# Kernel optimization log

Measured on AMD Instinct MI355X. Metric: run time of the kernel, lower is better.

Reference implementation:

```python
import jax, jax.numpy as jnp
import numpy as np

E, H, I, B, K = 8, 2048, 5632, 1024, 2


def setup_inputs() -> dict:
    key = jax.random.key(0)
    k_x, k_id, k_w, k_g, k_u, k_d = jax.random.split(key, 6)
    x = jax.random.normal(k_x, (B, H), dtype=jnp.float32)
    expert_ids = jax.random.randint(k_id, (B, K), 0, E).astype(jnp.int32)
    ew = jax.random.uniform(k_w, (B, K), dtype=jnp.float32)
    expert_weights = ew / jnp.sum(ew, axis=-1, keepdims=True)  # router probs, sum to 1
    scale = 0.02
    gate_weights = jax.random.normal(k_g, (E, H, I), dtype=jnp.float32) * scale
    up_weights = jax.random.normal(k_u, (E, H, I), dtype=jnp.float32) * scale
    down_weights = jax.random.normal(k_d, (E, I, H), dtype=jnp.float32) * scale
    return {
        "x": x,
        "expert_ids": expert_ids,
        "expert_weights": expert_weights,
        "gate_weights": gate_weights,
        "up_weights": up_weights,
        "down_weights": down_weights,
    }


def reference(x, expert_ids, expert_weights, gate_weights, up_weights, down_weights):
    # Faithful math: per token t, expert e = expert_ids[t,k]:
    #   out[t] = sum_k expert_weights[t,k] * (silu(x W_gate_e) * (x W_up_e)) W_down_e
    # Implemented as dense all-expert GEMMs + select, which computes the
    # identical per-expert matmuls as the original's gathered-weight einsums
    # without materializing the [B,K,H,I] gathered weight tensor.
    gate_all = jnp.einsum('bh,ehi->bei', x, gate_weights)        # [B,E,I]
    up_all = jnp.einsum('bh,ehi->bei', x, up_weights)            # [B,E,I]
    act_all = jax.nn.silu(gate_all) * up_all                     # [B,E,I]
    out_all = jnp.einsum('bei,eih->beh', act_all, down_weights)  # [B,E,H]
    # Select the top_k experts' outputs per token: [B,K,H]
    sel = jnp.take_along_axis(out_all, expert_ids[:, :, None], axis=1)
    return jnp.sum(sel * expert_weights[:, :, None], axis=1)     # [B,H]
```

## Files before the change

kernel.cpp:

```cpp
#include <hip/hip_runtime.h>
#include <hip/hip_bf16.h>

#define E_ 8
#define H_ 2048
#define I_ 5632
#define B_ 1024
#define K_ 2
#define NROWS (B_*K_)

#define BM 128
#define BN 64
#define BK 64
#define MAXT 24
#define NKG (H_/BK)
#define NKD (I_/BK)
#define NYG (I_/BN)
#define NYD (H_/BN)

typedef __attribute__((ext_vector_type(8))) __bf16 bf16x8;
typedef __attribute__((ext_vector_type(4))) float f32x4;

union BF4 { __bf16 b[4]; uint2 q; };
union BF8 { __bf16 b[8]; uint4 q; };

__device__ __forceinline__ void gld_lds16(const void* g, void* l) {
  __builtin_amdgcn_global_load_lds(
      (const __attribute__((address_space(1))) void*)g,
      (__attribute__((address_space(3))) void*)l, 16, 0, 0);
}

#define GLOAD4(dst, ptr) asm volatile("global_load_dwordx4 %0, %1, off" : "=v"(dst) : "v"(ptr))
#define WAITV(N) do { asm volatile("s_waitcnt vmcnt(" #N ")" ::: "memory"); __builtin_amdgcn_sched_barrier(0); } while(0)
#define WAITL()  do { asm volatile("s_waitcnt lgkmcnt(0)" ::: "memory"); __builtin_amdgcn_sched_barrier(0); } while(0)
#define BAR()    __builtin_amdgcn_s_barrier()

#define MSK(c) (((c)&7) ^ (((c)>>2)&7))

__global__ void cvtx_kernel(const float* __restrict__ x, __bf16* __restrict__ xb) {
  int i = (blockIdx.x * 256 + threadIdx.x) * 8;
  float4 a = *(const float4*)(x + i);
  float4 b = *(const float4*)(x + i + 4);
  BF8 r;
  r.b[0] = (__bf16)a.x; r.b[1] = (__bf16)a.y; r.b[2] = (__bf16)a.z; r.b[3] = (__bf16)a.w;
  r.b[4] = (__bf16)b.x; r.b[5] = (__bf16)b.y; r.b[6] = (__bf16)b.z; r.b[7] = (__bf16)b.w;
  *(uint4*)(xb + i) = r.q;
}

__global__ void route_kernel(const int* __restrict__ ids,
                             int* __restrict__ counts, int* __restrict__ offsets,
                             int* __restrict__ tlist, int* __restrict__ row_of,
                             int* __restrict__ tile_e, int* __restrict__ tile_m) {
  __shared__ int sc[E_], sp[E_], so[E_];
  int t = threadIdx.x;
  if (t < E_) { sc[t] = 0; sp[t] = 0; }
  __syncthreads();
  for (int idx = t; idx < NROWS; idx += 256) atomicAdd(&sc[ids[idx]], 1);
  __syncthreads();
  if (t == 0) {
    int acc = 0;
    for (int e = 0; e < E_; ++e) { so[e] = acc; acc += sc[e]; }
    int nt = 0;
    for (int e = 0; e < E_; ++e)
      for (int m0 = 0; m0 < sc[e]; m0 += BM) { tile_e[nt] = e; tile_m[nt] = m0; ++nt; }
    for (; nt < MAXT; ++nt) { tile_e[nt] = 0; tile_m[nt] = 0x7FFFFFFF; }
  }
  __syncthreads();
  for (int idx = t; idx < NROWS; idx += 256) {
    int e = ids[idx];
    int slot = atomicAdd(&sp[e], 1);
    int row = so[e] + slot;
    tlist[row] = idx / K_;
    row_of[idx] = row;
  }
  if (t < E_) { counts[t] = sc[t]; offsets[t] = so[t]; }
}

__global__ __launch_bounds__(256, 2) void gateup_kernel(
    const __bf16* __restrict__ xb, const float* __restrict__ gw,
    const float* __restrict__ uw, const int* __restrict__ counts,
    const int* __restrict__ offsets, const int* __restrict__ tlist,
    const int* __restrict__ tile_e, const int* __restrict__ tile_m,
    __bf16* __restrict__ act)
{
  extern __shared__ char smem[];
  char* As0 = smem;
  char* As1 = smem + 16384;
  char* Bg0 = smem + 32768;
  char* Bg1 = smem + 40960;
  char* Bu0 = smem + 49152;
  char* Bu1 = smem + 57344;

  const int id = blockIdx.x;
  const int w  = (id & 7) * 264 + (id >> 3);
  const int tt = w % MAXT;
  const int ny = w / MAXT;
  const int e  = tile_e[tt];
  const int m0 = tile_m[tt];
  const int cnt = counts[e];
  if (m0 >= cnt) return;
  const int off = offsets[e];
  const int n0 = ny * BN;

  const int tid  = threadIdx.x;
  const int lane = tid & 63;
  const int wave = tid >> 6;
  const int wr = (wave >> 1) * 64;
  const int wc = (wave & 1) * 32;

  const __bf16* asrc0; const __bf16* asrc1; const __bf16* asrc2; const __bf16* asrc3;
  int ad0, ad1, ad2, ad3;
  {
    const __bf16* s[4]; int d[4];
#pragma unroll
    for (int i = 0; i < 4; ++i) {
      int f = i*256 + tid;
      int r = f >> 3, cs = f & 7;
      int rr = m0 + r; if (rr >= cnt) rr = cnt - 1;
      int tok = tlist[off + rr];
      s[i] = xb + (size_t)tok * H_ + ((cs ^ (r & 7)) << 3);
      d[i] = f * 16;
    }
    asrc0=s[0]; asrc1=s[1]; asrc2=s[2]; asrc3=s[3];
    ad0=d[0]; ad1=d[1]; ad2=d[2]; ad3=d[3];
  }

  const int cq = tid & 15;
  const int kb = (tid >> 4) * 4;
  const float* pg0 = gw + ((size_t)e*H_ + kb + 0)*I_ + n0 + 4*cq;
  const float* pg1 = gw + ((size_t)e*H_ + kb + 1)*I_ + n0 + 4*cq;
  const float* pg2 = gw + ((size_t)e*H_ + kb + 2)*I_ + n0 + 4*cq;
  const float* pg3 = gw + ((size_t)e*H_ + kb + 3)*I_ + n0 + 4*cq;
  const float* pu0 = uw + ((size_t)e*H_ + kb + 0)*I_ + n0 + 4*cq;
  const float* pu1 = uw + ((size_t)e*H_ + kb + 1)*I_ + n0 + 4*cq;
  const float* pu2 = uw + ((size_t)e*H_ + kb + 2)*I_ + n0 + 4*cq;
  const float* pu3 = uw + ((size_t)e*H_ + kb + 3)*I_ + n0 + 4*cq;
  const int slot = kb >> 3;
  const int half = (kb & 4) << 1;
  int bw0, bw1, bw2, bw3;
  {
    int b[4];
#pragma unroll
    for (int i = 0; i < 4; ++i) {
      int c = 4*cq + i;
      b[i] = c*128 + ((slot ^ MSK(c)) << 4) + half;
    }
    bw0=b[0]; bw1=b[1]; bw2=b[2]; bw3=b[3];
  }

  f32x4 vgA_0,vgA_1,vgA_2,vgA_3, vuA_0,vuA_1,vuA_2,vuA_3;
  f32x4 vgB_0,vgB_1,vgB_2,vgB_3, vuB_0,vuB_1,vuB_2,vuB_3;

  f32x4 accg[4][2], accu[4][2];
#pragma unroll
  for (int i = 0; i < 4; ++i)
#pragma unroll
    for (int j = 0; j < 2; ++j) {
      accg[i][j] = (f32x4){0.f,0.f,0.f,0.f};
      accu[i][j] = (f32x4){0.f,0.f,0.f,0.f};
    }

  auto COMPUTE = [&](const char* Ab, const char* Bgb, const char* Bub) {
#pragma unroll
    for (int kk = 0; kk < 2; ++kk) {
      const int ks = kk*4 + (lane >> 4);
      const int r0 = wr + (lane & 15);
      const int swa = (ks ^ (r0 & 7)) << 4;
      bf16x8 a0 = *(const bf16x8*)(Ab + (r0 +  0)*128 + swa);
      bf16x8 a1 = *(const bf16x8*)(Ab + (r0 + 16)*128 + swa);
      bf16x8 a2 = *(const bf16x8*)(Ab + (r0 + 32)*128 + swa);
      bf16x8 a3 = *(const bf16x8*)(Ab + (r0 + 48)*128 + swa);
      const int c0 = wc + (lane & 15);
      const int swb0 = (ks ^ MSK(c0)) << 4;
      const int swb1 = swb0 ^ (4 << 4);
      bf16x8 g0 = *(const bf16x8*)(Bgb + c0*128 + swb0);
      bf16x8 g1 = *(const bf16x8*)(Bgb + (c0+16)*128 + swb1);
      bf16x8 u0 = *(const bf16x8*)(Bub + c0*128 + swb0);
      bf16x8 u1 = *(const bf16x8*)(Bub + (c0+16)*128 + swb1);
      accg[0][0] = __builtin_amdgcn_mfma_f32_16x16x32_bf16(a0, g0, accg[0][0], 0,0,0);
      accg[1][0] = __builtin_amdgcn_mfma_f32_16x16x32_bf16(a1, g0, accg[1][0], 0,0,0);
      accg[2][0] = __builtin_amdgcn_mfma_f32_16x16x32_bf16(a2, g0, accg[2][0], 0,0,0);
      accg[3][0] = __builtin_amdgcn_mfma_f32_16x16x32_bf16(a3, g0, accg[3][0], 0,0,0);
      accg[0][1] = __builtin_amdgcn_mfma_f32_16x16x32_bf16(a0, g1, accg[0][1], 0,0,0);
      accg[1][1] = __builtin_amdgcn_mfma_f32_16x16x32_bf16(a1, g1, accg[1][1], 0,0,0);
      accg[2][1] = __builtin_amdgcn_mfma_f32_16x16x32_bf16(a2, g1, accg[2][1], 0,0,0);
      accg[3][1] = __builtin_amdgcn_mfma_f32_16x16x32_bf16(a3, g1, accg[3][1], 0,0,0);
      accu[0][0] = __builtin_amdgcn_mfma_f32_16x16x32_bf16(a0, u0, accu[0][0], 0,0,0);
      accu[1][0] = __builtin_amdgcn_mfma_f32_16x16x32_bf16(a1, u0, accu[1][0], 0,0,0);
      accu[2][0] = __builtin_amdgcn_mfma_f32_16x16x32_bf16(a2, u0, accu[2][0], 0,0,0);
      accu[3][0] = __builtin_amdgcn_mfma_f32_16x16x32_bf16(a3, u0, accu[3][0], 0,0,0);
      accu[0][1] = __builtin_amdgcn_mfma_f32_16x16x32_bf16(a0, u1, accu[0][1], 0,0,0);
      accu[1][1] = __builtin_amdgcn_mfma_f32_16x16x32_bf16(a1, u1, accu[1][1], 0,0,0);
      accu[2][1] = __builtin_amdgcn_mfma_f32_16x16x32_bf16(a2, u1, accu[2][1], 0,0,0);
      accu[3][1] = __builtin_amdgcn_mfma_f32_16x16x32_bf16(a3, u1, accu[3][1], 0,0,0);
    }
  };

#define GU_PF(S, KPF) do { size_t o_ = (size_t)(KPF)*(size_t)BK*(size_t)I_; \
    GLOAD4(vg##S##_0, pg0+o_); GLOAD4(vu##S##_0, pu0+o_); \
    GLOAD4(vg##S##_1, pg1+o_); GLOAD4(vu##S##_1, pu1+o_); \
    GLOAD4(vg##S##_2, pg2+o_); GLOAD4(vu##S##_2, pu2+o_); \
    GLOAD4(vg##S##_3, pg3+o_); GLOAD4(vu##S##_3, pu3+o_); } while(0)

#define GU_CVW1(BG, V0, V1, V2, V3, BWI, I) do { BF4 p_; \
    p_.b[0]=(__bf16)V0[I]; p_.b[1]=(__bf16)V1[I]; p_.b[2]=(__bf16)V2[I]; p_.b[3]=(__bf16)V3[I]; \
    *(uint2*)((BG)+BWI) = p_.q; } while(0)

#define GU_CVW(S, BG, BU) do { \
    GU_CVW1(BG, vg##S##_0, vg##S##_1, vg##S##_2, vg##S##_3, bw0, 0); \
    GU_CVW1(BG, vg##S##_0, vg##S##_1, vg##S##_2, vg##S##_3, bw1, 1); \
    GU_CVW1(BG, vg##S##_0, vg##S##_1, vg##S##_2, vg##S##_3, bw2, 2); \
    GU_CVW1(BG, vg##S##_0, vg##S##_1, vg##S##_2, vg##S##_3, bw3, 3); \
    GU_CVW1(BU, vu##S##_0, vu##S##_1, vu##S##_2, vu##S##_3, bw0, 0); \
    GU_CVW1(BU, vu##S##_0, vu##S##_1, vu##S##_2, vu##S##_3, bw1, 1); \
    GU_CVW1(BU, vu##S##_0, vu##S##_1, vu##S##_2, vu##S##_3, bw2, 2); \
    GU_CVW1(BU, vu##S##_0, vu##S##_1, vu##S##_2, vu##S##_3, bw3, 3); } while(0)

#define GU_GLDA(DST, KPF) do { size_t k_ = (size_t)(KPF)*(size_t)BK; \
    gld_lds16(asrc0 + k_, (DST)+ad0); gld_lds16(asrc1 + k_, (DST)+ad1); \
    gld_lds16(asrc2 + k_, (DST)+ad2); gld_lds16(asrc3 + k_, (DST)+ad3); } while(0)

  GU_PF(A, 0);
  GU_GLDA(As0, 0);
  WAITV(4);
  GU_CVW(A, Bg0, Bu0);
  GU_PF(B, 1);
  GU_GLDA(As1, 1);
  WAITV(12);
  WAITL();
  BAR();

#pragma unroll 1
  for (int kt = 0; kt < NKG; kt += 2) {
    {
      int kpf = kt + 2; if (kpf > NKG-1) kpf = NKG-1;
      GU_PF(A, kpf);
      COMPUTE(As0, Bg0, Bu0);
      WAITV(12);
      GU_CVW(B, Bg1, Bu1);
      WAITV(8);
      WAITL();
      BAR();
      GU_GLDA(As0, kpf);
    }
    {
      int kpf = kt + 3; if (kpf > NKG-1) kpf = NKG-1;
      GU_PF(B, kpf);
      COMPUTE(As1, Bg1, Bu1);
      WAITV(12);
      GU_CVW(A, Bg0, Bu0);
      WAITV(8);
      WAITL();
      BAR();
      GU_GLDA(As1, kpf);
    }
  }
  WAITV(0);
  WAITL();

  const int rsub = (lane >> 4) * 4;
  const int csub = lane & 15;
#pragma unroll
  for (int mi = 0; mi < 4; ++mi)
#pragma unroll
    for (int j = 0; j < 4; ++j) {
      int rl = wr + mi*16 + rsub + j;
      if (m0 + rl < cnt) {
        size_t orow = (size_t)(off + m0 + rl) * I_ + n0 + wc + csub;
#pragma unroll
        for (int cg = 0; cg < 2; ++cg) {
          float g = accg[mi][cg][j];
          float u = accu[mi][cg][j];
          float sg = g / (1.0f + __expf(-g));
          act[orow + cg*16] = (__bf16)(sg * u);
        }
      }
    }
#undef GU_PF
#undef GU_CVW
#undef GU_CVW1
#undef GU_GLDA
}

__global__ __launch_bounds__(256, 3) void down_kernel(
    const __bf16* __restrict__ act, const float* __restrict__ dw,
    const int* __restrict__ counts, const int* __restrict__ offsets,
    const int* __restrict__ tile_e, const int* __restrict__ tile_m,
    float* __restrict__ rowbuf)
{
  extern __shared__ char smem[];
  char* As0 = smem;
  char* As1 = smem + 16384;
  char* Bs0 = smem + 32768;
  char* Bs1 = smem + 40960;

  const int id = blockIdx.x;
  const int w  = (id & 7) * 96 + (id >> 3);
  const int tt = w % MAXT;
  const int ny = w / MAXT;
  const int e  = tile_e[tt];
  const int m0 = tile_m[tt];
  const int cnt = counts[e];
  if (m0 >= cnt) return;
  const int off = offsets[e];
  const int n0 = ny * BN;

  const int tid  = threadIdx.x;
  const int lane = tid & 63;
  const int wave = tid >> 6;
  const int wr = (wave >> 1) * 64;
  const int wc = (wave & 1) * 32;

  const __bf16* asrc0; const __bf16* asrc1; const __bf16* asrc2; const __bf16* asrc3;
  int ad0, ad1, ad2, ad3;
  {
    const __bf16* s[4]; int d[4];
#pragma unroll
    for (int i = 0; i < 4; ++i) {
      int f = i*256 + tid;
      int r = f >> 3, cs = f & 7;
      int rr = m0 + r; if (rr >= cnt) rr = cnt - 1;
      s[i] = act + (size_t)(off + rr) * I_ + ((cs ^ (r & 7)) << 3);
      d[i] = f * 16;
    }
    asrc0=s[0]; asrc1=s[1]; asrc2=s[2]; asrc3=s[3];
    ad0=d[0]; ad1=d[1]; ad2=d[2]; ad3=d[3];
  }

  const int cq = tid & 15;
  const int kb = (tid >> 4) * 4;
  const float* pd0 = dw + ((size_t)e*I_ + kb + 0)*H_ + n0 + 4*cq;
  const float* pd1 = dw + ((size_t)e*I_ + kb + 1)*H_ + n0 + 4*cq;
  const float* pd2 = dw + ((size_t)e*I_ + kb + 2)*H_ + n0 + 4*cq;
  const float* pd3 = dw + ((size_t)e*I_ + kb + 3)*H_ + n0 + 4*cq;
  const int slot = kb >> 3;
  const int half = (kb & 4) << 1;
  int bw0, bw1, bw2, bw3;
  {
    int b[4];
#pragma unroll
    for (int i = 0; i < 4; ++i) {
      int c = 4*cq + i;
      b[i] = c*128 + ((slot ^ MSK(c)) << 4) + half;
    }
    bw0=b[0]; bw1=b[1]; bw2=b[2]; bw3=b[3];
  }

  f32x4 vdA_0,vdA_1,vdA_2,vdA_3;
  f32x4 vdB_0,vdB_1,vdB_2,vdB_3;

  f32x4 acc[4][2];
#pragma unroll
  for (int i = 0; i < 4; ++i)
#pragma unroll
    for (int j = 0; j < 2; ++j) acc[i][j] = (f32x4){0.f,0.f,0.f,0.f};

  auto COMPUTE = [&](const char* Ab, const char* Bb) {
#pragma unroll
    for (int kk = 0; kk < 2; ++kk) {
      const int ks = kk*4 + (lane >> 4);
      const int r0 = wr + (lane & 15);
      const int swa = (ks ^ (r0 & 7)) << 4;
      bf16x8 a0 = *(const bf16x8*)(Ab + (r0 +  0)*128 + swa);
      bf16x8 a1 = *(const bf16x8*)(Ab + (r0 + 16)*128 + swa);
      bf16x8 a2 = *(const bf16x8*)(Ab + (r0 + 32)*128 + swa);
      bf16x8 a3 = *(const bf16x8*)(Ab + (r0 + 48)*128 + swa);
      const int c0 = wc + (lane & 15);
      const int swb0 = (ks ^ MSK(c0)) << 4;
      const int swb1 = swb0 ^ (4 << 4);
      bf16x8 b0 = *(const bf16x8*)(Bb + c0*128 + swb0);
      bf16x8 b1 = *(const bf16x8*)(Bb + (c0+16)*128 + swb1);
      acc[0][0] = __builtin_amdgcn_mfma_f32_16x16x32_bf16(a0, b0, acc[0][0], 0,0,0);
      acc[1][0] = __builtin_amdgcn_mfma_f32_16x16x32_bf16(a1, b0, acc[1][0], 0,0,0);
      acc[2][0] = __builtin_amdgcn_mfma_f32_16x16x32_bf16(a2, b0, acc[2][0], 0,0,0);
      acc[3][0] = __builtin_amdgcn_mfma_f32_16x16x32_bf16(a3, b0, acc[3][0], 0,0,0);
      acc[0][1] = __builtin_amdgcn_mfma_f32_16x16x32_bf16(a0, b1, acc[0][1], 0,0,0);
      acc[1][1] = __builtin_amdgcn_mfma_f32_16x16x32_bf16(a1, b1, acc[1][1], 0,0,0);
      acc[2][1] = __builtin_amdgcn_mfma_f32_16x16x32_bf16(a2, b1, acc[2][1], 0,0,0);
      acc[3][1] = __builtin_amdgcn_mfma_f32_16x16x32_bf16(a3, b1, acc[3][1], 0,0,0);
    }
  };

#define DN_PF(S, KPF) do { size_t o_ = (size_t)(KPF)*(size_t)BK*(size_t)H_; \
    GLOAD4(vd##S##_0, pd0+o_); GLOAD4(vd##S##_1, pd1+o_); \
    GLOAD4(vd##S##_2, pd2+o_); GLOAD4(vd##S##_3, pd3+o_); } while(0)

#define DN_CVW1(BB, V0, V1, V2, V3, BWI, I) do { BF4 p_; \
    p_.b[0]=(__bf16)V0[I]; p_.b[1]=(__bf16)V1[I]; p_.b[2]=(__bf16)V2[I]; p_.b[3]=(__bf16)V3[I]; \
    *(uint2*)((BB)+BWI) = p_.q; } while(0)

#define DN_CVW(S, BB) do { \
    DN_CVW1(BB, vd##S##_0, vd##S##_1, vd##S##_2, vd##S##_3, bw0, 0); \
    DN_CVW1(BB, vd##S##_0, vd##S##_1, vd##S##_2, vd##S##_3, bw1, 1); \
    DN_CVW1(BB, vd##S##_0, vd##S##_1, vd##S##_2, vd##S##_3, bw2, 2); \
    DN_CVW1(BB, vd##S##_0, vd##S##_1, vd##S##_2, vd##S##_3, bw3, 3); } while(0)

#define DN_GLDA(DST, KPF) do { size_t k_ = (size_t)(KPF)*(size_t)BK; \
    gld_lds16(asrc0 + k_, (DST)+ad0); gld_lds16(asrc1 + k_, (DST)+ad1); \
    gld_lds16(asrc2 + k_, (DST)+ad2); gld_lds16(asrc3 + k_, (DST)+ad3); } while(0)

  DN_PF(A, 0);
  DN_GLDA(As0, 0);
  WAITV(4);
  DN_CVW(A, Bs0);
  DN_PF(B, 1);
  DN_GLDA(As1, 1);
  WAITV(8);
  WAITL();
  BAR();

#pragma unroll 1
  for (int kt = 0; kt < NKD; kt += 2) {
    {
      int kpf = kt + 2; if (kpf > NKD-1) kpf = NKD-1;
      DN_PF(A, kpf);
      COMPUTE(As0, Bs0);
      WAITV(8);
      DN_CVW(B, Bs1);
      WAITV(4);
      WAITL();
      BAR();
      DN_GLDA(As0, kpf);
    }
    {
      int kpf = kt + 3; if (kpf > NKD-1) kpf = NKD-1;
      DN_PF(B, kpf);
      COMPUTE(As1, Bs1);
      WAITV(8);
      DN_CVW(A, Bs0);
      WAITV(4);
      WAITL();
      BAR();
      DN_GLDA(As1, kpf);
    }
  }
  WAITV(0);
  WAITL();

  const int rsub = (lane >> 4) * 4;
  const int csub = lane & 15;
#pragma unroll
  for (int mi = 0; mi < 4; ++mi)
#pragma unroll
    for (int j = 0; j < 4; ++j) {
      int rl = wr + mi*16 + rsub + j;
      if (m0 + rl < cnt) {
        size_t orow = (size_t)(off + m0 + rl) * H_ + n0 + wc + csub;
#pragma unroll
        for (int cg = 0; cg < 2; ++cg)
          rowbuf[orow + cg*16] = acc[mi][cg][j];
      }
    }
#undef DN_PF
#undef DN_CVW
#undef DN_CVW1
#undef DN_GLDA
}

__global__ void combine_kernel(const float* __restrict__ ew, const int* __restrict__ row_of,
                               const float* __restrict__ rowbuf, float* __restrict__ out) {
  int idx = blockIdx.x * 256 + threadIdx.x;
  int t  = idx >> 9;
  int h4 = idx & 511;
  float w0 = ew[t*2+0], w1 = ew[t*2+1];
  int r0 = row_of[t*2+0], r1 = row_of[t*2+1];
  float4 a = *(const float4*)(rowbuf + (size_t)r0*H_ + h4*4);
  float4 b = *(const float4*)(rowbuf + (size_t)r1*H_ + h4*4);
  float4 o;
  o.x = w0*a.x + w1*b.x; o.y = w0*a.y + w1*b.y;
  o.z = w0*a.z + w1*b.z; o.w = w0*a.w + w1*b.w;
  *(float4*)(out + (size_t)idx*4) = o;
}

extern "C" void kernel_launch(void* const* d_in, const int* in_sizes, int n_in,
                              void* d_out, int out_size, void* d_ws, size_t ws_size,
                              hipStream_t stream) {
  const float* x   = (const float*)d_in[0];
  const int*   ids = (const int*)d_in[1];
  const float* ew  = (const float*)d_in[2];
  const float* gw  = (const float*)d_in[3];
  const float* uw  = (const float*)d_in[4];
  const float* dwn = (const float*)d_in[5];
  float* out = (float*)d_out;

  char* ws = (char*)d_ws;
  int* counts  = (int*)ws;
  int* offsets = counts + 8;
  int* tlist   = offsets + 8;
  int* row_of  = tlist + NROWS;
  int* tile_e  = row_of + NROWS;
  int* tile_m  = tile_e + MAXT;
  __bf16* xb   = (__bf16*)(ws + 32768);
  __bf16* act  = (__bf16*)(ws + 32768 + (size_t)B_*H_*2);
  float* rowbuf = (float*)(ws + 32768 + (size_t)B_*H_*2 + (size_t)NROWS*I_*2);

  hipFuncSetAttribute(reinterpret_cast<const void*>(&gateup_kernel),
                      hipFuncAttributeMaxDynamicSharedMemorySize, 65536);
  hipFuncSetAttribute(reinterpret_cast<const void*>(&down_kernel),
                      hipFuncAttributeMaxDynamicSharedMemorySize, 49152);

  cvtx_kernel<<<B_*H_/(256*8), 256, 0, stream>>>(x, xb);
  route_kernel<<<1, 256, 0, stream>>>(ids, counts, offsets, tlist, row_of, tile_e, tile_m);

  gateup_kernel<<<MAXT*NYG, 256, 65536, stream>>>(xb, gw, uw, counts, offsets, tlist,
                                                  tile_e, tile_m, act);

  down_kernel<<<MAXT*NYD, 256, 49152, stream>>>(act, dwn, counts, offsets,
                                                tile_e, tile_m, rowbuf);

  combine_kernel<<<(B_*H_/4)/256, 256, 0, stream>>>(ew, row_of, rowbuf, out);
}
```

Baseline: 415.1 us.

## Load A fragments directly into registers and narrow gate/up tile width

```diff
diff --git a/kernel.cpp b/kernel.cpp
--- a/kernel.cpp
+++ b/kernel.cpp
@@ -9,30 +9,25 @@
 #define NROWS (B_*K_)
 
 #define BM 128
-#define BN 64
 #define BK 64
 #define MAXT 24
 #define NKG (H_/BK)
 #define NKD (I_/BK)
-#define NYG (I_/BN)
-#define NYD (H_/BN)
+#define NYG (I_/32)
+#define NYD (H_/64)
 
 typedef __attribute__((ext_vector_type(8))) __bf16 bf16x8;
 typedef __attribute__((ext_vector_type(4))) float f32x4;
 
+union BF2 { __bf16 b[2]; uint q; };
 union BF4 { __bf16 b[4]; uint2 q; };
 union BF8 { __bf16 b[8]; uint4 q; };
-
-__device__ __forceinline__ void gld_lds16(const void* g, void* l) {
-  __builtin_amdgcn_global_load_lds(
-      (const __attribute__((address_space(1))) void*)g,
-      (__attribute__((address_space(3))) void*)l, 16, 0, 0);
-}
 
 #define GLOAD4(dst, ptr) asm volatile("global_load_dwordx4 %0, %1, off" : "=v"(dst) : "v"(ptr))
 #define WAITV(N) do { asm volatile("s_waitcnt vmcnt(" #N ")" ::: "memory"); __builtin_amdgcn_sched_barrier(0); } while(0)
 #define WAITL()  do { asm volatile("s_waitcnt lgkmcnt(0)" ::: "memory"); __builtin_amdgcn_sched_barrier(0); } while(0)
 #define BAR()    __builtin_amdgcn_s_barrier()
+#define SB0()    __builtin_amdgcn_sched_barrier(0)
 
 #define MSK(c) (((c)&7) ^ (((c)>>2)&7))
 
@@ -83,15 +78,13 @@
     __bf16* __restrict__ act)
 {
   extern __shared__ char smem[];
-  char* As0 = smem;
-  char* As1 = smem + 16384;
-  char* Bg0 = smem + 32768;
-  char* Bg1 = smem + 40960;
-  char* Bu0 = smem + 49152;
-  char* Bu1 = smem + 57344;
+  char* Bg0 = smem;
+  char* Bg1 = smem + 4096;
+  char* Bu0 = smem + 8192;
+  char* Bu1 = smem + 12288;
 
   const int id = blockIdx.x;
-  const int w  = (id & 7) * 264 + (id >> 3);
+  const int w  = (id & 7) * 528 + (id >> 3);
   const int tt = w % MAXT;
   const int ny = w / MAXT;
   const int e  = tile_e[tt];
@@ -99,133 +92,120 @@
   const int cnt = counts[e];
   if (m0 >= cnt) return;
   const int off = offsets[e];
-  const int n0 = ny * BN;
+  const int n0 = ny * 32;
 
   const int tid  = threadIdx.x;
   const int lane = tid & 63;
   const int wave = tid >> 6;
   const int wr = (wave >> 1) * 64;
-  const int wc = (wave & 1) * 32;
-
-  const __bf16* asrc0; const __bf16* asrc1; const __bf16* asrc2; const __bf16* asrc3;
-  int ad0, ad1, ad2, ad3;
+  const int wc = (wave & 1) * 16;
+
+  const __bf16* ab0; const __bf16* ab1; const __bf16* ab2; const __bf16* ab3;
   {
-    const __bf16* s[4]; int d[4];
-#pragma unroll
-    for (int i = 0; i < 4; ++i) {
-      int f = i*256 + tid;
-      int r = f >> 3, cs = f & 7;
-      int rr = m0 + r; if (rr >= cnt) rr = cnt - 1;
+    const __bf16* a[4];
+#pragma unroll
+    for (int mi = 0; mi < 4; ++mi) {
+      int rr = m0 + wr + mi*16 + (lane & 15);
+      if (rr >= cnt) rr = cnt - 1;
       int tok = tlist[off + rr];
-      s[i] = xb + (size_t)tok * H_ + ((cs ^ (r & 7)) << 3);
-      d[i] = f * 16;
-    }
-    asrc0=s[0]; asrc1=s[1]; asrc2=s[2]; asrc3=s[3];
-    ad0=d[0]; ad1=d[1]; ad2=d[2]; ad3=d[3];
-  }
-
-  const int cq = tid & 15;
-  const int kb = (tid >> 4) * 4;
-  const float* pg0 = gw + ((size_t)e*H_ + kb + 0)*I_ + n0 + 4*cq;
-  const float* pg1 = gw + ((size_t)e*H_ + kb + 1)*I_ + n0 + 4*cq;
-  const float* pg2 = gw + ((size_t)e*H_ + kb + 2)*I_ + n0 + 4*cq;
-  const float* pg3 = gw + ((size_t)e*H_ + kb + 3)*I_ + n0 + 4*cq;
-  const float* pu0 = uw + ((size_t)e*H_ + kb + 0)*I_ + n0 + 4*cq;
-  const float* pu1 = uw + ((size_t)e*H_ + kb + 1)*I_ + n0 + 4*cq;
-  const float* pu2 = uw + ((size_t)e*H_ + kb + 2)*I_ + n0 + 4*cq;
-  const float* pu3 = uw + ((size_t)e*H_ + kb + 3)*I_ + n0 + 4*cq;
-  const int slot = kb >> 3;
-  const int half = (kb & 4) << 1;
+      a[mi] = xb + (size_t)tok * H_ + ((lane >> 4) * 8);
+    }
+    ab0=a[0]; ab1=a[1]; ab2=a[2]; ab3=a[3];
+  }
+
+  const int q  = tid & 7;
+  const int kr = tid >> 3;
+  const int kb = kr * 2;
+  const float* pg0 = gw + ((size_t)e*H_ + kb + 0)*I_ + n0 + 4*q;
+  const float* pg1 = gw + ((size_t)e*H_ + kb + 1)*I_ + n0 + 4*q;
+  const float* pu0 = uw + ((size_t)e*H_ + kb + 0)*I_ + n0 + 4*q;
+  const float* pu1 = uw + ((size_t)e*H_ + kb + 1)*I_ + n0 + 4*q;
+  const int slot = kr >> 2;
+  const int insl = (kr & 3) * 4;
   int bw0, bw1, bw2, bw3;
   {
     int b[4];
 #pragma unroll
     for (int i = 0; i < 4; ++i) {
-      int c = 4*cq + i;
-      b[i] = c*128 + ((slot ^ MSK(c)) << 4) + half;
+      int c = 4*q + i;
+      b[i] = c*128 + ((slot ^ MSK(c)) << 4) + insl;
     }
     bw0=b[0]; bw1=b[1]; bw2=b[2]; bw3=b[3];
   }
 
-  f32x4 vgA_0,vgA_1,vgA_2,vgA_3, vuA_0,vuA_1,vuA_2,vuA_3;
-  f32x4 vgB_0,vgB_1,vgB_2,vgB_3, vuB_0,vuB_1,vuB_2,vuB_3;
-
-  f32x4 accg[4][2], accu[4][2];
-#pragma unroll
-  for (int i = 0; i < 4; ++i)
-#pragma unroll
-    for (int j = 0; j < 2; ++j) {
-      accg[i][j] = (f32x4){0.f,0.f,0.f,0.f};
-      accu[i][j] = (f32x4){0.f,0.f,0.f,0.f};
-    }
-
-  auto COMPUTE = [&](const char* Ab, const char* Bgb, const char* Bub) {
-#pragma unroll
-    for (int kk = 0; kk < 2; ++kk) {
-      const int ks = kk*4 + (lane >> 4);
-      const int r0 = wr + (lane & 15);
-      const int swa = (ks ^ (r0 & 7)) << 4;
-      bf16x8 a0 = *(const bf16x8*)(Ab + (r0 +  0)*128 + swa);
-      bf16x8 a1 = *(const bf16x8*)(Ab + (r0 + 16)*128 + swa);
-      bf16x8 a2 = *(const bf16x8*)(Ab + (r0 + 32)*128 + swa);
-      bf16x8 a3 = *(const bf16x8*)(Ab + (r0 + 48)*128 + swa);
+  f32x4 vgA_0,vgA_1, vuA_0,vuA_1;
+  f32x4 vgB_0,vgB_1, vuB_0,vuB_1;
+  bf16x8 tA_0,tA_1,tA_2,tA_3,tA_4,tA_5,tA_6,tA_7;
+
+  f32x4 accg[4], accu[4];
+#pragma unroll
+  for (int i = 0; i < 4; ++i) {
+    accg[i] = (f32x4){0.f,0.f,0.f,0.f};
+    accu[i] = (f32x4){0.f,0.f,0.f,0.f};
+  }
+
+  auto COMPUTE = [&](const char* Bgp, const char* Bup) {
+    {
+      const int ks = (lane >> 4);
       const int c0 = wc + (lane & 15);
-      const int swb0 = (ks ^ MSK(c0)) << 4;
-      const int swb1 = swb0 ^ (4 << 4);
-      bf16x8 g0 = *(const bf16x8*)(Bgb + c0*128 + swb0);
-      bf16x8 g1 = *(const bf16x8*)(Bgb + (c0+16)*128 + swb1);
-      bf16x8 u0 = *(const bf16x8*)(Bub + c0*128 + swb0);
-      bf16x8 u1 = *(const bf16x8*)(Bub + (c0+16)*128 + swb1);
-      accg[0][0] = __builtin_amdgcn_mfma_f32_16x16x32_bf16(a0, g0, accg[0][0], 0,0,0);
-      accg[1][0] = __builtin_amdgcn_mfma_f32_16x16x32_bf16(a1, g0, accg[1][0], 0,0,0);
-      accg[2][0] = __builtin_amdgcn_mfma_f32_16x16x32_bf16(a2, g0, accg[2][0], 0,0,0);
-      accg[3][0] = __builtin_amdgcn_mfma_f32_16x16x32_bf16(a3, g0, accg[3][0], 0,0,0);
-      accg[0][1] = __builtin_amdgcn_mfma_f32_16x16x32_bf16(a0, g1, accg[0][1], 0,0,0);
-      accg[1][1] = __builtin_amdgcn_mfma_f32_16x16x32_bf16(a1, g1, accg[1][1], 0,0,0);
-      accg[2][1] = __builtin_amdgcn_mfma_f32_16x16x32_bf16(a2, g1, accg[2][1], 0,0,0);
-      accg[3][1] = __builtin_amdgcn_mfma_f32_16x16x32_bf16(a3, g1, accg[3][1], 0,0,0);
-      accu[0][0] = __builtin_amdgcn_mfma_f32_16x16x32_bf16(a0, u0, accu[0][0], 0,0,0);
-      accu[1][0] = __builtin_amdgcn_mfma_f32_16x16x32_bf16(a1, u0, accu[1][0], 0,0,0);
-      accu[2][0] = __builtin_amdgcn_mfma_f32_16x16x32_bf16(a2, u0, accu[2][0], 0,0,0);
-      accu[3][0] = __builtin_amdgcn_mfma_f32_16x16x32_bf16(a3, u0, accu[3][0], 0,0,0);
-      accu[0][1] = __builtin_amdgcn_mfma_f32_16x16x32_bf16(a0, u1, accu[0][1], 0,0,0);
-      accu[1][1] = __builtin_amdgcn_mfma_f32_16x16x32_bf16(a1, u1, accu[1][1], 0,0,0);
-      accu[2][1] = __builtin_amdgcn_mfma_f32_16x16x32_bf16(a2, u1, accu[2][1], 0,0,0);
-      accu[3][1] = __builtin_amdgcn_mfma_f32_16x16x32_bf16(a3, u1, accu[3][1], 0,0,0);
+      const int swb = (ks ^ MSK(c0)) << 4;
+      bf16x8 g0 = *(const bf16x8*)(Bgp + c0*128 + swb);
+      bf16x8 u0 = *(const bf16x8*)(Bup + c0*128 + swb);
+      accg[0] = __builtin_amdgcn_mfma_f32_16x16x32_bf16(tA_0, g0, accg[0], 0,0,0);
+      accg[1] = __builtin_amdgcn_mfma_f32_16x16x32_bf16(tA_1, g0, accg[1], 0,0,0);
+      accg[2] = __builtin_amdgcn_mfma_f32_16x16x32_bf16(tA_2, g0, accg[2], 0,0,0);
+      accg[3] = __builtin_amdgcn_mfma_f32_16x16x32_bf16(tA_3, g0, accg[3], 0,0,0);
+      accu[0] = __builtin_amdgcn_mfma_f32_16x16x32_bf16(tA_0, u0, accu[0], 0,0,0);
+      accu[1] = __builtin_amdgcn_mfma_f32_16x16x32_bf16(tA_1, u0, accu[1], 0,0,0);
+      accu[2] = __builtin_amdgcn_mfma_f32_16x16x32_bf16(tA_2, u0, accu[2], 0,0,0);
+      accu[3] = __builtin_amdgcn_mfma_f32_16x16x32_bf16(tA_3, u0, accu[3], 0,0,0);
+    }
+    {
+      const int ks = 4 + (lane >> 4);
+      const int c0 = wc + (lane & 15);
+      const int swb = (ks ^ MSK(c0)) << 4;
+      bf16x8 g1 = *(const bf16x8*)(Bgp + c0*128 + swb);
+      bf16x8 u1 = *(const bf16x8*)(Bup + c0*128 + swb);
+      accg[0] = __builtin_amdgcn_mfma_f32_16x16x32_bf16(tA_4, g1, accg[0], 0,0,0);
+      accg[1] = __builtin_amdgcn_mfma_f32_16x16x32_bf16(tA_5, g1, accg[1], 0,0,0);
+      accg[2] = __builtin_amdgcn_mfma_f32_16x16x32_bf16(tA_6, g1, accg[2], 0,0,0);
+      accg[3] = __builtin_amdgcn_mfma_f32_16x16x32_bf16(tA_7, g1, accg[3], 0,0,0);
+      accu[0] = __builtin_amdgcn_mfma_f32_16x16x32_bf16(tA_4, u1, accu[0], 0,0,0);
+      accu[1] = __builtin_amdgcn_mfma_f32_16x16x32_bf16(tA_5, u1, accu[1], 0,0,0);
+      accu[2] = __builtin_amdgcn_mfma_f32_16x16x32_bf16(tA_6, u1, accu[2], 0,0,0);
+      accu[3] = __builtin_amdgcn_mfma_f32_16x16x32_bf16(tA_7, u1, accu[3], 0,0,0);
     }
   };
 
 #define GU_PF(S, KPF) do { size_t o_ = (size_t)(KPF)*(size_t)BK*(size_t)I_; \
-    GLOAD4(vg##S##_0, pg0+o_); GLOAD4(vu##S##_0, pu0+o_); \
-    GLOAD4(vg##S##_1, pg1+o_); GLOAD4(vu##S##_1, pu1+o_); \
-    GLOAD4(vg##S##_2, pg2+o_); GLOAD4(vu##S##_2, pu2+o_); \
-    GLOAD4(vg##S##_3, pg3+o_); GLOAD4(vu##S##_3, pu3+o_); } while(0)
-
-#define GU_CVW1(BG, V0, V1, V2, V3, BWI, I) do { BF4 p_; \
-    p_.b[0]=(__bf16)V0[I]; p_.b[1]=(__bf16)V1[I]; p_.b[2]=(__bf16)V2[I]; p_.b[3]=(__bf16)V3[I]; \
-    *(uint2*)((BG)+BWI) = p_.q; } while(0)
+    GLOAD4(vg##S##_0, pg0+o_); GLOAD4(vg##S##_1, pg1+o_); \
+    GLOAD4(vu##S##_0, pu0+o_); GLOAD4(vu##S##_1, pu1+o_); } while(0)
+
+#define GU_CVW1(BB, V0, V1, BWI, I) do { BF2 p_; \
+    p_.b[0]=(__bf16)V0[I]; p_.b[1]=(__bf16)V1[I]; \
+    *(uint*)((BB)+BWI) = p_.q; } while(0)
 
 #define GU_CVW(S, BG, BU) do { \
-    GU_CVW1(BG, vg##S##_0, vg##S##_1, vg##S##_2, vg##S##_3, bw0, 0); \
-    GU_CVW1(BG, vg##S##_0, vg##S##_1, vg##S##_2, vg##S##_3, bw1, 1); \
-    GU_CVW1(BG, vg##S##_0, vg##S##_1, vg##S##_2, vg##S##_3, bw2, 2); \
-    GU_CVW1(BG, vg##S##_0, vg##S##_1, vg##S##_2, vg##S##_3, bw3, 3); \
-    GU_CVW1(BU, vu##S##_0, vu##S##_1, vu##S##_2, vu##S##_3, bw0, 0); \
-    GU_CVW1(BU, vu##S##_0, vu##S##_1, vu##S##_2, vu##S##_3, bw1, 1); \
-    GU_CVW1(BU, vu##S##_0, vu##S##_1, vu##S##_2, vu##S##_3, bw2, 2); \
-    GU_CVW1(BU, vu##S##_0, vu##S##_1, vu##S##_2, vu##S##_3, bw3, 3); } while(0)
-
-#define GU_GLDA(DST, KPF) do { size_t k_ = (size_t)(KPF)*(size_t)BK; \
-    gld_lds16(asrc0 + k_, (DST)+ad0); gld_lds16(asrc1 + k_, (DST)+ad1); \
-    gld_lds16(asrc2 + k_, (DST)+ad2); gld_lds16(asrc3 + k_, (DST)+ad3); } while(0)
+    GU_CVW1(BG, vg##S##_0, vg##S##_1, bw0, 0); \
+    GU_CVW1(BG, vg##S##_0, vg##S##_1, bw1, 1); \
+    GU_CVW1(BG, vg##S##_0, vg##S##_1, bw2, 2); \
+    GU_CVW1(BG, vg##S##_0, vg##S##_1, bw3, 3); \
+    GU_CVW1(BU, vu##S##_0, vu##S##_1, bw0, 0); \
+    GU_CVW1(BU, vu##S##_0, vu##S##_1, bw1, 1); \
+    GU_CVW1(BU, vu##S##_0, vu##S##_1, bw2, 2); \
+    GU_CVW1(BU, vu##S##_0, vu##S##_1, bw3, 3); } while(0)
+
+#define APF(KT) do { size_t e0_ = (size_t)(KT)*64; \
+    GLOAD4(tA_0, ab0 + e0_);      GLOAD4(tA_1, ab1 + e0_); \
+    GLOAD4(tA_2, ab2 + e0_);      GLOAD4(tA_3, ab3 + e0_); \
+    GLOAD4(tA_4, ab0 + e0_ + 32); GLOAD4(tA_5, ab1 + e0_ + 32); \
+    GLOAD4(tA_6, ab2 + e0_ + 32); GLOAD4(tA_7, ab3 + e0_ + 32); } while(0)
 
   GU_PF(A, 0);
-  GU_GLDA(As0, 0);
-  WAITV(4);
+  WAITV(0);
   GU_CVW(A, Bg0, Bu0);
   GU_PF(B, 1);
-  GU_GLDA(As1, 1);
-  WAITV(12);
+  APF(0);
   WAITL();
   BAR();
 
@@ -234,24 +214,25 @@
     {
       int kpf = kt + 2; if (kpf > NKG-1) kpf = NKG-1;
       GU_PF(A, kpf);
-      COMPUTE(As0, Bg0, Bu0);
-      WAITV(12);
+      WAITV(4);
+      COMPUTE(Bg0, Bu0);
       GU_CVW(B, Bg1, Bu1);
-      WAITV(8);
+      SB0();
+      APF(kt + 1);
       WAITL();
       BAR();
-      GU_GLDA(As0, kpf);
     }
     {
       int kpf = kt + 3; if (kpf > NKG-1) kpf = NKG-1;
+      int ka  = kt + 2; if (ka  > NKG-1) ka  = NKG-1;
       GU_PF(B, kpf);
-      COMPUTE(As1, Bg1, Bu1);
-      WAITV(12);
+      WAITV(4);
+      COMPUTE(Bg1, Bu1);
       GU_CVW(A, Bg0, Bu0);
-      WAITV(8);
+      SB0();
+      APF(ka);
       WAITL();
       BAR();
-      GU_GLDA(As1, kpf);
     }
   }
   WAITV(0);
@@ -266,32 +247,27 @@
       int rl = wr + mi*16 + rsub + j;
       if (m0 + rl < cnt) {
         size_t orow = (size_t)(off + m0 + rl) * I_ + n0 + wc + csub;
-#pragma unroll
-        for (int cg = 0; cg < 2; ++cg) {
-          float g = accg[mi][cg][j];
-          float u = accu[mi][cg][j];
-          float sg = g / (1.0f + __expf(-g));
-          act[orow + cg*16] = (__bf16)(sg * u);
-        }
+        float g = accg[mi][j];
+        float u = accu[mi][j];
+        float sg = g / (1.0f + __expf(-g));
+        act[orow] = (__bf16)(sg * u);
       }
     }
 #undef GU_PF
 #undef GU_CVW
 #undef GU_CVW1
-#undef GU_GLDA
-}
-
-__global__ __launch_bounds__(256, 3) void down_kernel(
+#undef APF
+}
+
+__global__ __launch_bounds__(256, 2) void down_kernel(
     const __bf16* __restrict__ act, const float* __restrict__ dw,
     const int* __restrict__ counts, const int* __restrict__ offsets,
     const int* __restrict__ tile_e, const int* __restrict__ tile_m,
     float* __restrict__ rowbuf)
 {
   extern __shared__ char smem[];
-  char* As0 = smem;
-  char* As1 = smem + 16384;
-  char* Bs0 = smem + 32768;
-  char* Bs1 = smem + 40960;
+  char* Bs0 = smem;
+  char* Bs1 = smem + 8192;
 
   const int id = blockIdx.x;
   const int w  = (id & 7) * 96 + (id >> 3);
@@ -302,7 +278,7 @@
   const int cnt = counts[e];
   if (m0 >= cnt) return;
   const int off = offsets[e];
-  const int n0 = ny * BN;
+  const int n0 = ny * 64;
 
   const int tid  = threadIdx.x;
   const int lane = tid & 63;
@@ -310,20 +286,16 @@
   const int wr = (wave >> 1) * 64;
   const int wc = (wave & 1) * 32;
 
-  const __bf16* asrc0; const __bf16* asrc1; const __bf16* asrc2; const __bf16* asrc3;
-  int ad0, ad1, ad2, ad3;
+  const __bf16* ab0; const __bf16* ab1; const __bf16* ab2; const __bf16* ab3;
   {
-    const __bf16* s[4]; int d[4];
-#pragma unroll
-    for (int i = 0; i < 4; ++i) {
-      int f = i*256 + tid;
-      int r = f >> 3, cs = f & 7;
-      int rr = m0 + r; if (rr >= cnt) rr = cnt - 1;
-      s[i] = act + (size_t)(off + rr) * I_ + ((cs ^ (r & 7)) << 3);
-      d[i] = f * 16;
-    }
-    asrc0=s[0]; asrc1=s[1]; asrc2=s[2]; asrc3=s[3];
-    ad0=d[0]; ad1=d[1]; ad2=d[2]; ad3=d[3];
+    const __bf16* a[4];
+#pragma unroll
+    for (int mi = 0; mi < 4; ++mi) {
+      int rr = m0 + wr + mi*16 + (lane & 15);
+      if (rr >= cnt) rr = cnt - 1;
+      a[mi] = act + (size_t)(off + rr) * I_ + ((lane >> 4) * 8);
+    }
+    ab0=a[0]; ab1=a[1]; ab2=a[2]; ab3=a[3];
   }
 
   const int cq = tid & 15;
@@ -347,6 +319,7 @@
 
   f32x4 vdA_0,vdA_1,vdA_2,vdA_3;
   f32x4 vdB_0,vdB_1,vdB_2,vdB_3;
+  bf16x8 tA_0,tA_1,tA_2,tA_3,tA_4,tA_5,tA_6,tA_7;
 
   f32x4 acc[4][2];
 #pragma unroll
@@ -354,29 +327,38 @@
 #pragma unroll
     for (int j = 0; j < 2; ++j) acc[i][j] = (f32x4){0.f,0.f,0.f,0.f};
 
-  auto COMPUTE = [&](const char* Ab, const char* Bb) {
-#pragma unroll
-    for (int kk = 0; kk < 2; ++kk) {
-      const int ks = kk*4 + (lane >> 4);
-      const int r0 = wr + (lane & 15);
-      const int swa = (ks ^ (r0 & 7)) << 4;
-      bf16x8 a0 = *(const bf16x8*)(Ab + (r0 +  0)*128 + swa);
-      bf16x8 a1 = *(const bf16x8*)(Ab + (r0 + 16)*128 + swa);
-      bf16x8 a2 = *(const bf16x8*)(Ab + (r0 + 32)*128 + swa);
-      bf16x8 a3 = *(const bf16x8*)(Ab + (r0 + 48)*128 + swa);
+  auto COMPUTE = [&](const char* Bp) {
+    {
+      const int ks = (lane >> 4);
       const int c0 = wc + (lane & 15);
       const int swb0 = (ks ^ MSK(c0)) << 4;
       const int swb1 = swb0 ^ (4 << 4);
-      bf16x8 b0 = *(const bf16x8*)(Bb + c0*128 + swb0);
-      bf16x8 b1 = *(const bf16x8*)(Bb + (c0+16)*128 + swb1);
-      acc[0][0] = __builtin_amdgcn_mfma_f32_16x16x32_bf16(a0, b0, acc[0][0], 0,0,0);
-      acc[1][0] = __builtin_amdgcn_mfma_f32_16x16x32_bf16(a1, b0, acc[1][0], 0,0,0);
-      acc[2][0] = __builtin_amdgcn_mfma_f32_16x16x32_bf16(a2, b0, acc[2][0], 0,0,0);
-      acc[3][0] = __builtin_amdgcn_mfma_f32_16x16x32_bf16(a3, b0, acc[3][0], 0,0,0);
-      acc[0][1] = __builtin_amdgcn_mfma_f32_16x16x32_bf16(a0, b1, acc[0][1], 0,0,0);
-      acc[1][1] = __builtin_amdgcn_mfma_f32_16x16x32_bf16(a1, b1, acc[1][1], 0,0,0);
-      acc[2][1] = __builtin_amdgcn_mfma_f32_16x16x32_bf16(a2, b1, acc[2][1], 0,0,0);
-      acc[3][1] = __builtin_amdgcn_mfma_f32_16x16x32_bf16(a3, b1, acc[3][1], 0,0,0);
+      bf16x8 b0 = *(const bf16x8*)(Bp + c0*128 + swb0);
+      bf16x8 b1 = *(const bf16x8*)(Bp + (c0+16)*128 + swb1);
+      acc[0][0] = __builtin_amdgcn_mfma_f32_16x16x32_bf16(tA_0, b0, acc[0][0], 0,0,0);
+      acc[1][0] = __builtin_amdgcn_mfma_f32_16x16x32_bf16(tA_1, b0, acc[1][0], 0,0,0);
+      acc[2][0] = __builtin_amdgcn_mfma_f32_16x16x32_bf16(tA_2, b0, acc[2][0], 0,0,0);
+      acc[3][0] = __builtin_amdgcn_mfma_f32_16x16x32_bf16(tA_3, b0, acc[3][0], 0,0,0);
+      acc[0][1] = __builtin_amdgcn_mfma_f32_16x16x32_bf16(tA_0, b1, acc[0][1], 0,0,0);
+      acc[1][1] = __builtin_amdgcn_mfma_f32_16x16x32_bf16(tA_1, b1, acc[1][1], 0,0,0);
+      acc[2][1] = __builtin_amdgcn_mfma_f32_16x16x32_bf16(tA_2, b1, acc[2][1], 0,0,0);
+      acc[3][1] = __builtin_amdgcn_mfma_f32_16x16x32_bf16(tA_3, b1, acc[3][1], 0,0,0);
+    }
+    {
+      const int ks = 4 + (lane >> 4);
+      const int c0 = wc + (lane & 15);
+      const int swb0 = (ks ^ MSK(c0)) << 4;
+      const int swb1 = swb0 ^ (4 << 4);
+      bf16x8 b0 = *(const bf16x8*)(Bp + c0*128 + swb0);
+      bf16x8 b1 = *(const bf16x8*)(Bp + (c0+16)*128 + swb1);
+      acc[0][0] = __builtin_amdgcn_mfma_f32_16x16x32_bf16(tA_4, b0, acc[0][0], 0,0,0);
+      acc[1][0] = __builtin_amdgcn_mfma_f32_16x16x32_bf16(tA_5, b0, acc[1][0], 0,0,0);
+      acc[2][0] = __builtin_amdgcn_mfma_f32_16x16x32_bf16(tA_6, b0, acc[2][0], 0,0,0);
+      acc[3][0] = __builtin_amdgcn_mfma_f32_16x16x32_bf16(tA_7, b0, acc[3][0], 0,0,0);
+      acc[0][1] = __builtin_amdgcn_mfma_f32_16x16x32_bf16(tA_4, b1, acc[0][1], 0,0,0);
+      acc[1][1] = __builtin_amdgcn_mfma_f32_16x16x32_bf16(tA_5, b1, acc[1][1], 0,0,0);
+      acc[2][1] = __builtin_amdgcn_mfma_f32_16x16x32_bf16(tA_6, b1, acc[2][1], 0,0,0);
+      acc[3][1] = __builtin_amdgcn_mfma_f32_16x16x32_bf16(tA_7, b1, acc[3][1], 0,0,0);
     }
   };
 
@@ -394,17 +376,17 @@
     DN_CVW1(BB, vd##S##_0, vd##S##_1, vd##S##_2, vd##S##_3, bw2, 2); \
     DN_CVW1(BB, vd##S##_0, vd##S##_1, vd##S##_2, vd##S##_3, bw3, 3); } while(0)
 
-#define DN_GLDA(DST, KPF) do { size_t k_ = (size_t)(KPF)*(size_t)BK; \
-    gld_lds16(asrc0 + k_, (DST)+ad0); gld_lds16(asrc1 + k_, (DST)+ad1); \
-    gld_lds16(asrc2 + k_, (DST)+ad2); gld_lds16(asrc3 + k_, (DST)+ad3); } while(0)
+#define APF(KT) do { size_t e0_ = (size_t)(KT)*64; \
+    GLOAD4(tA_0, ab0 + e0_);      GLOAD4(tA_1, ab1 + e0_); \
+    GLOAD4(tA_2, ab2 + e0_);      GLOAD4(tA_3, ab3 + e0_); \
+    GLOAD4(tA_4, ab0 + e0_ + 32); GLOAD4(tA_5, ab1 + e0_ + 32); \
+    GLOAD4(tA_6, ab2 + e0_ + 32); GLOAD4(tA_7, ab3 + e0_ + 32); } while(0)
 
   DN_PF(A, 0);
-  DN_GLDA(As0, 0);
-  WAITV(4);
+  WAITV(0);
   DN_CVW(A, Bs0);
   DN_PF(B, 1);
-  DN_GLDA(As1, 1);
-  WAITV(8);
+  APF(0);
   WAITL();
   BAR();
 
@@ -413,24 +395,25 @@
     {
       int kpf = kt + 2; if (kpf > NKD-1) kpf = NKD-1;
       DN_PF(A, kpf);
-      COMPUTE(As0, Bs0);
-      WAITV(8);
+      WAITV(4);
+      COMPUTE(Bs0);
       DN_CVW(B, Bs1);
-      WAITV(4);
+      SB0();
+      APF(kt + 1);
       WAITL();
       BAR();
-      DN_GLDA(As0, kpf);
     }
     {
       int kpf = kt + 3; if (kpf > NKD-1) kpf = NKD-1;
+      int ka  = kt + 2; if (ka  > NKD-1) ka  = NKD-1;
       DN_PF(B, kpf);
-      COMPUTE(As1, Bs1);
-      WAITV(8);
+      WAITV(4);
+      COMPUTE(Bs1);
       DN_CVW(A, Bs0);
-      WAITV(4);
+      SB0();
+      APF(ka);
       WAITL();
       BAR();
-      DN_GLDA(As1, kpf);
     }
   }
   WAITV(0);
@@ -453,7 +436,7 @@
 #undef DN_PF
 #undef DN_CVW
 #undef DN_CVW1
-#undef DN_GLDA
+#undef APF
 }
 
 __global__ void combine_kernel(const float* __restrict__ ew, const int* __restrict__ row_of,
@@ -494,17 +477,17 @@
   float* rowbuf = (float*)(ws + 32768 + (size_t)B_*H_*2 + (size_t)NROWS*I_*2);
 
   hipFuncSetAttribute(reinterpret_cast<const void*>(&gateup_kernel),
-                      hipFuncAttributeMaxDynamicSharedMemorySize, 65536);
+                      hipFuncAttributeMaxDynamicSharedMemorySize, 16384);
   hipFuncSetAttribute(reinterpret_cast<const void*>(&down_kernel),
-                      hipFuncAttributeMaxDynamicSharedMemorySize, 49152);
+                      hipFuncAttributeMaxDynamicSharedMemorySize, 16384);
 
   cvtx_kernel<<<B_*H_/(256*8), 256, 0, stream>>>(x, xb);
   route_kernel<<<1, 256, 0, stream>>>(ids, counts, offsets, tlist, row_of, tile_e, tile_m);
 
-  gateup_kernel<<<MAXT*NYG, 256, 65536, stream>>>(xb, gw, uw, counts, offsets, tlist,
+  gateup_kernel<<<MAXT*NYG, 256, 16384, stream>>>(xb, gw, uw, counts, offsets, tlist,
                                                   tile_e, tile_m, act);
 
-  down_kernel<<<MAXT*NYD, 256, 49152, stream>>>(act, dwn, counts, offsets,
+  down_kernel<<<MAXT*NYD, 256, 16384, stream>>>(act, dwn, counts, offsets,
                                                 tile_e, tile_m, rowbuf);
 
   combine_kernel<<<(B_*H_/4)/256, 256, 0, stream>>>(ew, row_of, rowbuf, out);
```

Measured after the change: 807.3 us. +94.5%, slower.

## Single-buffer A tile in gate/up kernel to fit three blocks per CU

Applied to the files above, without the earlier changes.

```diff
diff --git a/kernel.cpp b/kernel.cpp
--- a/kernel.cpp
+++ b/kernel.cpp
@@ -75,7 +75,7 @@
   if (t < E_) { counts[t] = sc[t]; offsets[t] = so[t]; }
 }
 
-__global__ __launch_bounds__(256, 2) void gateup_kernel(
+__global__ __launch_bounds__(256, 3) void gateup_kernel(
     const __bf16* __restrict__ xb, const float* __restrict__ gw,
     const float* __restrict__ uw, const int* __restrict__ counts,
     const int* __restrict__ offsets, const int* __restrict__ tlist,
@@ -83,12 +83,11 @@
     __bf16* __restrict__ act)
 {
   extern __shared__ char smem[];
-  char* As0 = smem;
-  char* As1 = smem + 16384;
-  char* Bg0 = smem + 32768;
-  char* Bg1 = smem + 40960;
-  char* Bu0 = smem + 49152;
-  char* Bu1 = smem + 57344;
+  char* As  = smem;
+  char* Bg0 = smem + 16384;
+  char* Bg1 = smem + 24576;
+  char* Bu0 = smem + 32768;
+  char* Bu1 = smem + 40960;
 
   const int id = blockIdx.x;
   const int w  = (id & 7) * 264 + (id >> 3);
@@ -159,16 +158,17 @@
       accu[i][j] = (f32x4){0.f,0.f,0.f,0.f};
     }
 
-  auto COMPUTE = [&](const char* Ab, const char* Bgb, const char* Bub) {
+  auto COMPUTE = [&](const char* Bgb, const char* Bub) {
+    __builtin_amdgcn_s_setprio(1);
 #pragma unroll
     for (int kk = 0; kk < 2; ++kk) {
       const int ks = kk*4 + (lane >> 4);
       const int r0 = wr + (lane & 15);
       const int swa = (ks ^ (r0 & 7)) << 4;
-      bf16x8 a0 = *(const bf16x8*)(Ab + (r0 +  0)*128 + swa);
-      bf16x8 a1 = *(const bf16x8*)(Ab + (r0 + 16)*128 + swa);
-      bf16x8 a2 = *(const bf16x8*)(Ab + (r0 + 32)*128 + swa);
-      bf16x8 a3 = *(const bf16x8*)(Ab + (r0 + 48)*128 + swa);
+      bf16x8 a0 = *(const bf16x8*)(As + (r0 +  0)*128 + swa);
+      bf16x8 a1 = *(const bf16x8*)(As + (r0 + 16)*128 + swa);
+      bf16x8 a2 = *(const bf16x8*)(As + (r0 + 32)*128 + swa);
+      bf16x8 a3 = *(const bf16x8*)(As + (r0 + 48)*128 + swa);
       const int c0 = wc + (lane & 15);
       const int swb0 = (ks ^ MSK(c0)) << 4;
       const int swb1 = swb0 ^ (4 << 4);
@@ -193,6 +193,7 @@
       accu[2][1] = __builtin_amdgcn_mfma_f32_16x16x32_bf16(a2, u1, accu[2][1], 0,0,0);
       accu[3][1] = __builtin_amdgcn_mfma_f32_16x16x32_bf16(a3, u1, accu[3][1], 0,0,0);
     }
+    __builtin_amdgcn_s_setprio(0);
   };
 
 #define GU_PF(S, KPF) do { size_t o_ = (size_t)(KPF)*(size_t)BK*(size_t)I_; \
@@ -215,17 +216,16 @@
     GU_CVW1(BU, vu##S##_0, vu##S##_1, vu##S##_2, vu##S##_3, bw2, 2); \
     GU_CVW1(BU, vu##S##_0, vu##S##_1, vu##S##_2, vu##S##_3, bw3, 3); } while(0)
 
-#define GU_GLDA(DST, KPF) do { size_t k_ = (size_t)(KPF)*(size_t)BK; \
-    gld_lds16(asrc0 + k_, (DST)+ad0); gld_lds16(asrc1 + k_, (DST)+ad1); \
-    gld_lds16(asrc2 + k_, (DST)+ad2); gld_lds16(asrc3 + k_, (DST)+ad3); } while(0)
+#define GU_GLDA(KPF) do { size_t k_ = (size_t)(KPF)*(size_t)BK; \
+    gld_lds16(asrc0 + k_, As+ad0); gld_lds16(asrc1 + k_, As+ad1); \
+    gld_lds16(asrc2 + k_, As+ad2); gld_lds16(asrc3 + k_, As+ad3); } while(0)
 
   GU_PF(A, 0);
-  GU_GLDA(As0, 0);
-  WAITV(4);
+  WAITV(0);
   GU_CVW(A, Bg0, Bu0);
+  GU_GLDA(0);
   GU_PF(B, 1);
-  GU_GLDA(As1, 1);
-  WAITV(12);
+  WAITV(8);
   WAITL();
   BAR();
 
@@ -233,25 +233,29 @@
   for (int kt = 0; kt < NKG; kt += 2) {
     {
       int kpf = kt + 2; if (kpf > NKG-1) kpf = NKG-1;
-      GU_PF(A, kpf);
-      COMPUTE(As0, Bg0, Bu0);
-      WAITV(12);
+      int ka  = kt + 1; if (ka  > NKG-1) ka  = NKG-1;
+      COMPUTE(Bg0, Bu0);
+      WAITV(0);
       GU_CVW(B, Bg1, Bu1);
-      WAITV(8);
       WAITL();
       BAR();
-      GU_GLDA(As0, kpf);
+      GU_GLDA(ka);
+      GU_PF(A, kpf);
+      WAITV(8);
+      BAR();
     }
     {
       int kpf = kt + 3; if (kpf > NKG-1) kpf = NKG-1;
-      GU_PF(B, kpf);
-      COMPUTE(As1, Bg1, Bu1);
-      WAITV(12);
+      int ka  = kt + 2; if (ka  > NKG-1) ka  = NKG-1;
+      COMPUTE(Bg1, Bu1);
+      WAITV(0);
       GU_CVW(A, Bg0, Bu0);
-      WAITV(8);
       WAITL();
       BAR();
-      GU_GLDA(As1, kpf);
+      GU_GLDA(ka);
+      GU_PF(B, kpf);
+      WAITV(8);
+      BAR();
     }
   }
   WAITV(0);
@@ -355,6 +359,7 @@
     for (int j = 0; j < 2; ++j) acc[i][j] = (f32x4){0.f,0.f,0.f,0.f};
 
   auto COMPUTE = [&](const char* Ab, const char* Bb) {
+    __builtin_amdgcn_s_setprio(1);
 #pragma unroll
     for (int kk = 0; kk < 2; ++kk) {
       const int ks = kk*4 + (lane >> 4);
@@ -378,6 +383,7 @@
       acc[2][1] = __builtin_amdgcn_mfma_f32_16x16x32_bf16(a2, b1, acc[2][1], 0,0,0);
       acc[3][1] = __builtin_amdgcn_mfma_f32_16x16x32_bf16(a3, b1, acc[3][1], 0,0,0);
     }
+    __builtin_amdgcn_s_setprio(0);
   };
 
 #define DN_PF(S, KPF) do { size_t o_ = (size_t)(KPF)*(size_t)BK*(size_t)H_; \
@@ -494,14 +500,14 @@
   float* rowbuf = (float*)(ws + 32768 + (size_t)B_*H_*2 + (size_t)NROWS*I_*2);
 
   hipFuncSetAttribute(reinterpret_cast<const void*>(&gateup_kernel),
-                      hipFuncAttributeMaxDynamicSharedMemorySize, 65536);
+                      hipFuncAttributeMaxDynamicSharedMemorySize, 49152);
   hipFuncSetAttribute(reinterpret_cast<const void*>(&down_kernel),
                       hipFuncAttributeMaxDynamicSharedMemorySize, 49152);
 
   cvtx_kernel<<<B_*H_/(256*8), 256, 0, stream>>>(x, xb);
   route_kernel<<<1, 256, 0, stream>>>(ids, counts, offsets, tlist, row_of, tile_e, tile_m);
 
-  gateup_kernel<<<MAXT*NYG, 256, 65536, stream>>>(xb, gw, uw, counts, offsets, tlist,
+  gateup_kernel<<<MAXT*NYG, 256, 49152, stream>>>(xb, gw, uw, counts, offsets, tlist,
                                                   tile_e, tile_m, act);
 
   down_kernel<<<MAXT*NYD, 256, 49152, stream>>>(act, dwn, counts, offsets,
```

Measured after the change: 428.8 us. 1.03x slower.
